# Optimization experiments

Hardware: AMD Instinct MI355X
Metric: run time of the kernel (lower is better)

Reference implementation:

```python
import jax, jax.numpy as jnp
import numpy as np

N_NODES = 5000
N_EDGES = 50000
HID = 64
OUT = 12
H, W = 12, 4
L = 3
BN_EPS = 1e-5
GEN_EPS = 1e-7


def setup_inputs() -> dict:
    key = jax.random.key(0)
    ks = jax.random.split(key, 12)
    node_feats = jax.random.normal(ks[0], (N_NODES, HID, H, W), dtype=jnp.float32)
    edge_feats = jax.random.normal(ks[1], (N_EDGES, HID, H, W), dtype=jnp.float32)
    src = jax.random.randint(ks[2], (N_EDGES,), 0, N_NODES)
    dst = jax.random.randint(ks[3], (N_EDGES,), 0, N_NODES)
    # per-layer params
    bn_gamma = jnp.ones((L, HID), dtype=jnp.float32)
    bn_beta = jnp.zeros((L, HID), dtype=jnp.float32)
    s = 1.0 / np.sqrt(HID)
    gen_W = jax.random.uniform(ks[4], (L, HID, HID), dtype=jnp.float32, minval=-s, maxval=s)
    gen_b = jax.random.uniform(ks[5], (L, HID), dtype=jnp.float32, minval=-s, maxval=s)
    out_W = jax.random.uniform(ks[6], (HID, OUT), dtype=jnp.float32, minval=-s, maxval=s)
    out_b = jax.random.uniform(ks[7], (OUT,), dtype=jnp.float32, minval=-s, maxval=s)
    return {
        "node_feats": node_feats, "edge_feats": edge_feats,
        "src": src, "dst": dst,
        "bn_gamma": bn_gamma, "bn_beta": bn_beta,
        "gen_W": gen_W, "gen_b": gen_b,
        "out_W": out_W, "out_b": out_b,
    }


def _batchnorm2d(x, gamma, beta):
    # training-mode BN over (N, H, W) per channel; x: [N, C, H, W]
    mu = jnp.mean(x, axis=(0, 2, 3), keepdims=True)
    var = jnp.mean((x - mu) ** 2, axis=(0, 2, 3), keepdims=True)
    xn = (x - mu) * jax.lax.rsqrt(var + BN_EPS)
    return xn * gamma[None, :, None, None] + beta[None, :, None, None]


def _genconv(h, he, src, dst, Wg, bg):
    # DeeperGCN GENConv with softmax aggregator (beta=1), mlp_layers=1.
    # h: [N, C, H, W], he: [E, C, H, W]
    m = jax.nn.relu(h[src] + he) + GEN_EPS                      # [E, C, H, W]
    mx = jax.ops.segment_max(m, dst, num_segments=N_NODES)      # [N, C, H, W]
    e = jnp.exp(m - mx[dst])
    s = jax.ops.segment_sum(e, dst, num_segments=N_NODES)
    a = e / s[dst]                                              # edge softmax per dst
    agg = jax.ops.segment_sum(a * m, dst, num_segments=N_NODES)
    feats = h + agg
    # linear over channel dim
    return jnp.einsum('nchw,co->nohw', feats, Wg) + bg[None, :, None, None]


def reference(node_feats, edge_feats, src, dst, bn_gamma, bn_beta, gen_W, gen_b, out_W, out_b):
    hv = node_feats
    he = edge_feats
    for l in range(L):
        hv1 = _batchnorm2d(hv, bn_gamma[l], bn_beta[l])
        hv1 = jax.nn.relu(hv1)  # dropout p=0.0 -> identity
        hv = _genconv(hv1, he, src, dst, gen_W[l], gen_b[l]) + hv
    # AvgPooling(g, hv.transpose(0,3)): mean over dim 0 of [W,C,H,N] == mean over W of hv
    h_g = jnp.mean(hv, axis=3, keepdims=True) * hv              # [N, C, H, W]
    out = jnp.einsum('nchw,co->nohw', h_g, out_W) + out_b[None, :, None, None]
    return out
```

## Files before the change

### kernel.cpp

```cpp
#include <hip/hip_runtime.h>
#include <float.h>

#define NN 5000
#define NE 50000
#define C 64
#define CHW4 768
#define SPLIT 25
#define NPS 200
#define MAXD 64

typedef float f32x4 __attribute__((ext_vector_type(4)));

__global__ void hist_kernel(const int* __restrict__ dst, int* __restrict__ cnt) {
  int e = blockIdx.x * 256 + threadIdx.x;
  if (e < NE) atomicAdd(&cnt[dst[e]], 1);
}

__global__ void scan_kernel(const int* __restrict__ cnt, int* __restrict__ off, int* __restrict__ cur) {
  __shared__ int tsum[256];
  int t = threadIdx.x;
  constexpr int PER = 20;
  int base = t * PER;
  int vals[PER];
  int local = 0;
#pragma unroll
  for (int i = 0; i < PER; i++) {
    int idx = base + i;
    int v = (idx < NN) ? cnt[idx] : 0;
    vals[i] = local;
    local += v;
  }
  tsum[t] = local;
  __syncthreads();
  for (int o = 1; o < 256; o <<= 1) {
    int v = (t >= o) ? tsum[t - o] : 0;
    __syncthreads();
    tsum[t] += v;
    __syncthreads();
  }
  int excl = (t == 0) ? 0 : tsum[t - 1];
#pragma unroll
  for (int i = 0; i < PER; i++) {
    int idx = base + i;
    if (idx < NN) {
      int o2 = excl + vals[i];
      off[idx] = o2;
      cur[idx] = o2;
    }
  }
  if (t == 255) off[NN] = excl + local;
}

__global__ void scatter_kernel(const int* __restrict__ dst, const int* __restrict__ src,
                               int* __restrict__ cur, int* __restrict__ eids, int* __restrict__ srcs) {
  int e = blockIdx.x * 256 + threadIdx.x;
  if (e < NE) {
    int p = atomicAdd(&cur[dst[e]], 1);
    eids[p] = e;
    srcs[p] = src[e];
  }
}

__global__ void bn_stats_kernel(const float* __restrict__ hv, float* __restrict__ statsN) {
  int c = blockIdx.x / SPLIT, s = blockIdx.x % SPLIT;
  int n0 = s * NPS;
  const float4* hv4 = (const float4*)hv;
  float sum = 0.f, ss = 0.f;
  for (int i = threadIdx.x; i < NPS * 12; i += 256) {
    int n = n0 + i / 12, p = i % 12;
    float4 v = hv4[(size_t)n * CHW4 + c * 12 + p];
    sum += v.x + v.y + v.z + v.w;
    ss += v.x * v.x + v.y * v.y + v.z * v.z + v.w * v.w;
  }
  __shared__ float rs[256], rq[256];
  rs[threadIdx.x] = sum;
  rq[threadIdx.x] = ss;
  __syncthreads();
  for (int o = 128; o > 0; o >>= 1) {
    if (threadIdx.x < o) {
      rs[threadIdx.x] += rs[threadIdx.x + o];
      rq[threadIdx.x] += rq[threadIdx.x + o];
    }
    __syncthreads();
  }
  if (threadIdx.x == 0) {
    int r = blockIdx.x & 7;
    atomicAdd(&statsN[r * 128 + c], rs[0]);
    atomicAdd(&statsN[r * 128 + 64 + c], rq[0]);
  }
}

__global__ void finalize2_kernel(const float* __restrict__ statsN, const float* __restrict__ gamma,
                                 const float* __restrict__ beta, float* __restrict__ sc,
                                 float* __restrict__ sh) {
  int c = threadIdx.x;
  if (c < C) {
    float s = 0.f, q = 0.f;
#pragma unroll
    for (int r = 0; r < 8; r++) {
      s += statsN[r * 128 + c];
      q += statsN[r * 128 + 64 + c];
    }
    const float inv = 1.f / 240000.f;
    float mu = s * inv;
    float var = q * inv - mu * mu;
    float scale = gamma[c] * rsqrtf(var + 1e-5f);
    sc[c] = scale;
    sh[c] = beta[c] - mu * scale;
  }
}

template <bool LAST>
__global__ __launch_bounds__(256) void aggregate_kernel(
    const float* __restrict__ hv, const float* __restrict__ he,
    const int* __restrict__ srcs, const int* __restrict__ eids, const int* __restrict__ off,
    const float* __restrict__ Wg, const float* __restrict__ bg,
    const float* __restrict__ sc, const float* __restrict__ sh,
    float* __restrict__ hvNext, float* __restrict__ statsNext,
    const float* __restrict__ oW, const float* __restrict__ ob,
    float* __restrict__ out) {
  __shared__ float Wl[4096];
  __shared__ float fl[3072];
  __shared__ float scl[64], shl[64];
  __shared__ int sE[MAXD], sS[MAXD];
  __shared__ float bsum[64], bsq[64];

  int n = blockIdx.x, t = threadIdx.x;
  for (int i = t; i < 4096; i += 256) Wl[i] = Wg[i];
  if (t < 64) {
    scl[t] = sc[t];
    shl[t] = sh[t];
    bsum[t] = 0.f;
    bsq[t] = 0.f;
  }
  __syncthreads();

  const float4* hv4 = (const float4*)hv;
  const f32x4* heV = (const f32x4*)he;

  float scv[3], shv[3], h1[12];
#pragma unroll
  for (int j = 0; j < 3; j++) {
    int q = t + j * 256;
    int c = q / 12;
    scv[j] = scl[c];
    shv[j] = shl[c];
    float4 v = hv4[(size_t)n * CHW4 + q];
    h1[4 * j + 0] = fmaxf(v.x * scv[j] + shv[j], 0.f);
    h1[4 * j + 1] = fmaxf(v.y * scv[j] + shv[j], 0.f);
    h1[4 * j + 2] = fmaxf(v.z * scv[j] + shv[j], 0.f);
    h1[4 * j + 3] = fmaxf(v.w * scv[j] + shv[j], 0.f);
  }

  float M[12], S[12], T[12];
#pragma unroll
  for (int i = 0; i < 12; i++) {
    M[i] = -FLT_MAX;
    S[i] = 0.f;
    T[i] = 0.f;
  }

  int e0 = off[n], d = off[n + 1] - e0;
  for (int base = 0; base < d; base += MAXD) {
    int cnt = min(MAXD, d - base);
    __syncthreads();
    if (t < cnt) {
      sE[t] = eids[e0 + base + t];
      sS[t] = srcs[e0 + base + t];
    }
    __syncthreads();
#pragma unroll 2
    for (int k = 0; k < cnt; k++) {
      size_t hb = (size_t)sS[k] * CHW4, eb = (size_t)sE[k] * CHW4;
#pragma unroll
      for (int j = 0; j < 3; j++) {
        int q = t + j * 256;
        float4 a = hv4[hb + q];
        f32x4 b = __builtin_nontemporal_load(&heV[eb + q]);
        float av[4] = {a.x, a.y, a.z, a.w};
        float bv[4] = {b.x, b.y, b.z, b.w};
#pragma unroll
        for (int u = 0; u < 4; u++) {
          float x = fmaxf(av[u] * scv[j] + shv[j], 0.f);
          float m = fmaxf(x + bv[u], 0.f) + 1e-7f;
          int idx = j * 4 + u;
          float dd = m - M[idx];
          float ed = __expf(-fabsf(dd));
          float f1 = dd > 0.f ? ed : 1.f;
          float f2 = dd > 0.f ? 1.f : ed;
          S[idx] = S[idx] * f1 + f2;
          T[idx] = T[idx] * f1 + f2 * m;
          M[idx] = fmaxf(M[idx], m);
        }
      }
    }
  }

  bool hasE = d > 0;
  float4* fl4 = (float4*)fl;
#pragma unroll
  for (int j = 0; j < 3; j++) {
    int q = t + j * 256, idx = 4 * j;
    float4 f;
    f.x = h1[idx + 0] + (hasE ? T[idx + 0] / S[idx + 0] : 0.f);
    f.y = h1[idx + 1] + (hasE ? T[idx + 1] / S[idx + 1] : 0.f);
    f.z = h1[idx + 2] + (hasE ? T[idx + 2] / S[idx + 2] : 0.f);
    f.w = h1[idx + 3] + (hasE ? T[idx + 3] / S[idx + 3] : 0.f);
    fl4[q] = f;
  }
  __syncthreads();

  int o0 = (t / 12) * 4, hbp = t % 12;
  float4 acc[4];
  if (t < 192) {
#pragma unroll
    for (int i = 0; i < 4; i++) {
      float bv = bg[o0 + i];
      acc[i] = make_float4(bv, bv, bv, bv);
    }
    const float4* w4 = (const float4*)Wl;
    int widx = o0 >> 2;
    for (int c2 = 0; c2 < 64; c2++) {
      float4 fv = fl4[c2 * 12 + hbp];
      float4 wv = w4[c2 * 16 + widx];
      acc[0].x += wv.x * fv.x; acc[0].y += wv.x * fv.y; acc[0].z += wv.x * fv.z; acc[0].w += wv.x * fv.w;
      acc[1].x += wv.y * fv.x; acc[1].y += wv.y * fv.y; acc[1].z += wv.y * fv.z; acc[1].w += wv.y * fv.w;
      acc[2].x += wv.z * fv.x; acc[2].y += wv.z * fv.y; acc[2].z += wv.z * fv.z; acc[2].w += wv.z * fv.w;
      acc[3].x += wv.w * fv.x; acc[3].y += wv.w * fv.y; acc[3].z += wv.w * fv.z; acc[3].w += wv.w * fv.w;
    }
#pragma unroll
    for (int i = 0; i < 4; i++) {
      float4 r = hv4[(size_t)n * CHW4 + (o0 + i) * 12 + hbp];
      acc[i].x += r.x; acc[i].y += r.y; acc[i].z += r.z; acc[i].w += r.w;
    }
  }

  if constexpr (!LAST) {
    if (t < 192) {
      float4* hn4 = (float4*)hvNext;
#pragma unroll
      for (int i = 0; i < 4; i++) {
        hn4[(size_t)n * CHW4 + (o0 + i) * 12 + hbp] = acc[i];
        float s4 = acc[i].x + acc[i].y + acc[i].z + acc[i].w;
        float q4 = acc[i].x * acc[i].x + acc[i].y * acc[i].y + acc[i].z * acc[i].z + acc[i].w * acc[i].w;
        atomicAdd(&bsum[o0 + i], s4);
        atomicAdd(&bsq[o0 + i], q4);
      }
    }
    __syncthreads();
    int r = n & 7;
    if (t < 64) atomicAdd(&statsNext[r * 128 + t], bsum[t]);
    else if (t < 128) atomicAdd(&statsNext[r * 128 + 64 + (t - 64)], bsq[t - 64]);
  } else {
    __syncthreads();
    if (t < 192) {
#pragma unroll
      for (int i = 0; i < 4; i++) fl4[(o0 + i) * 12 + hbp] = acc[i];
    }
    for (int i = t; i < 768; i += 256) Wl[i] = oW[i];
    __syncthreads();
    for (int i = t; i < 768; i += 256) {
      float4 v = fl4[i];
      Wl[1024 + i] = (v.x + v.y + v.z + v.w) * 0.25f;
    }
    __syncthreads();
    if (t < 144) {
      int o = t / 12, hb = t % 12;
      float bias = ob[o];
      float4 a = make_float4(bias, bias, bias, bias);
      for (int c2 = 0; c2 < 64; c2++) {
        float4 v = fl4[c2 * 12 + hb];
        float wv = Wl[c2 * 12 + o] * Wl[1024 + c2 * 12 + hb];
        a.x += wv * v.x; a.y += wv * v.y; a.z += wv * v.z; a.w += wv * v.w;
      }
      ((float4*)out)[(size_t)n * 144 + t] = a;
    }
  }
}

extern "C" void kernel_launch(void* const* d_in, const int* in_sizes, int n_in,
                              void* d_out, int out_size, void* d_ws, size_t ws_size,
                              hipStream_t stream) {
  const float* node_feats = (const float*)d_in[0];
  const float* edge_feats = (const float*)d_in[1];
  const int* src = (const int*)d_in[2];
  const int* dst = (const int*)d_in[3];
  const float* bn_gamma = (const float*)d_in[4];
  const float* bn_beta = (const float*)d_in[5];
  const float* gen_W = (const float*)d_in[6];
  const float* gen_b = (const float*)d_in[7];
  const float* out_W = (const float*)d_in[8];
  const float* out_b = (const float*)d_in[9];
  float* out = (float*)d_out;

  char* ws = (char*)d_ws;
  float* hvA = (float*)ws;
  float* hvB = (float*)(ws + 61440000);
  float* statsN = (float*)(ws + 122880000);
  float* sc = (float*)(ws + 122884096);
  float* sh = (float*)(ws + 122884352);
  int* cnt = (int*)(ws + 122884608);
  int* off = (int*)(ws + 122904608);
  int* cur = (int*)(ws + 122924612);
  int* eids = (int*)(ws + 122944612);
  int* srcs = (int*)(ws + 123144612);

  hipMemsetAsync(cnt, 0, NN * sizeof(int), stream);
  hist_kernel<<<(NE + 255) / 256, 256, 0, stream>>>(dst, cnt);
  scan_kernel<<<1, 256, 0, stream>>>(cnt, off, cur);
  scatter_kernel<<<(NE + 255) / 256, 256, 0, stream>>>(dst, src, cur, eids, srcs);

  hipMemsetAsync(statsN, 0, 1024 * sizeof(float), stream);
  bn_stats_kernel<<<C * SPLIT, 256, 0, stream>>>(node_feats, statsN);

  const float* hvPrev = node_feats;
  float* bufs[2] = {hvA, hvB};
  for (int l = 0; l < 3; l++) {
    finalize2_kernel<<<1, 64, 0, stream>>>(statsN, bn_gamma + l * C, bn_beta + l * C, sc, sh);
    if (l < 2) {
      hipMemsetAsync(statsN, 0, 1024 * sizeof(float), stream);
      float* hvNext = bufs[l & 1];
      aggregate_kernel<false><<<NN, 256, 0, stream>>>(
          hvPrev, edge_feats, srcs, eids, off, gen_W + l * C * C, gen_b + l * C,
          sc, sh, hvNext, statsN, out_W, out_b, out);
      hvPrev = hvNext;
    } else {
      aggregate_kernel<true><<<NN, 256, 0, stream>>>(
          hvPrev, edge_feats, srcs, eids, off, gen_W + l * C * C, gen_b + l * C,
          sc, sh, hvA, statsN, out_W, out_b, out);
    }
  }
}
```

Baseline: 631.7 us.

## Store normalized node and sorted edge features in bf16, drop online-max softmax

Adds a per-layer kernel that applies BN+ReLU once per node and stores the result as bf16. Layer 0 also writes the edge features as bf16 in dst-sorted order, so layers 1 and 2 read them contiguously instead of gathering fp32 rows through eids. The softmax aggregation now accumulates exp(m) directly with no running max, which removes the rescaling arithmetic. The gathered traffic roughly halves, but bf16 rounding lowers precision and plain exp can overflow for large m. It also adds an extra full pass over node features and a large new workspace buffer.

```diff
diff --git a/kernel.cpp b/kernel.cpp
--- a/kernel.cpp
+++ b/kernel.cpp
@@ -10,6 +10,16 @@
 #define MAXD 64
 
 typedef float f32x4 __attribute__((ext_vector_type(4)));
+typedef unsigned int u32x2 __attribute__((ext_vector_type(2)));
+
+__device__ __forceinline__ unsigned int pack_bf16(float a, float b) {
+  unsigned int ua = __float_as_uint(a), ub = __float_as_uint(b);
+  ua = (ua + 0x7FFFu + ((ua >> 16) & 1u)) >> 16;
+  ub = (ub + 0x7FFFu + ((ub >> 16) & 1u)) & 0xFFFF0000u;
+  return ua | ub;
+}
+__device__ __forceinline__ float bf_lo(unsigned int u) { return __uint_as_float(u << 16); }
+__device__ __forceinline__ float bf_hi(unsigned int u) { return __uint_as_float(u & 0xFFFF0000u); }
 
 __global__ void hist_kernel(const int* __restrict__ dst, int* __restrict__ cnt) {
   int e = blockIdx.x * 256 + threadIdx.x;
@@ -110,9 +120,29 @@
   }
 }
 
-template <bool LAST>
+__global__ __launch_bounds__(256) void h1_kernel(const float* __restrict__ hv,
+                                                 const float* __restrict__ sc,
+                                                 const float* __restrict__ sh,
+                                                 u32x2* __restrict__ h1g) {
+  int idx = blockIdx.x * 256 + threadIdx.x;
+  int q = idx % CHW4;
+  int c = q / 12;
+  float s = sc[c], b = sh[c];
+  float4 v = ((const float4*)hv)[idx];
+  float x0 = fmaxf(v.x * s + b, 0.f);
+  float x1 = fmaxf(v.y * s + b, 0.f);
+  float x2 = fmaxf(v.z * s + b, 0.f);
+  float x3 = fmaxf(v.w * s + b, 0.f);
+  u32x2 o;
+  o.x = pack_bf16(x0, x1);
+  o.y = pack_bf16(x2, x3);
+  h1g[idx] = o;
+}
+
+template <bool FIRST, bool LAST>
 __global__ __launch_bounds__(256) void aggregate_kernel(
     const float* __restrict__ hv, const float* __restrict__ he,
+    const u32x2* __restrict__ h1g, u32x2* __restrict__ heb,
     const int* __restrict__ srcs, const int* __restrict__ eids, const int* __restrict__ off,
     const float* __restrict__ Wg, const float* __restrict__ bg,
     const float* __restrict__ sc, const float* __restrict__ sh,
@@ -122,7 +152,7 @@
   __shared__ float Wl[4096];
   __shared__ float fl[3072];
   __shared__ float scl[64], shl[64];
-  __shared__ int sE[MAXD], sS[MAXD];
+  __shared__ int sS[MAXD], sE[MAXD];
   __shared__ float bsum[64], bsq[64];
 
   int n = blockIdx.x, t = threadIdx.x;
@@ -138,24 +168,22 @@
   const float4* hv4 = (const float4*)hv;
   const f32x4* heV = (const f32x4*)he;
 
-  float scv[3], shv[3], h1[12];
+  float h1[12];
 #pragma unroll
   for (int j = 0; j < 3; j++) {
     int q = t + j * 256;
     int c = q / 12;
-    scv[j] = scl[c];
-    shv[j] = shl[c];
+    float s = scl[c], b = shl[c];
     float4 v = hv4[(size_t)n * CHW4 + q];
-    h1[4 * j + 0] = fmaxf(v.x * scv[j] + shv[j], 0.f);
-    h1[4 * j + 1] = fmaxf(v.y * scv[j] + shv[j], 0.f);
-    h1[4 * j + 2] = fmaxf(v.z * scv[j] + shv[j], 0.f);
-    h1[4 * j + 3] = fmaxf(v.w * scv[j] + shv[j], 0.f);
-  }
-
-  float M[12], S[12], T[12];
+    h1[4 * j + 0] = fmaxf(v.x * s + b, 0.f);
+    h1[4 * j + 1] = fmaxf(v.y * s + b, 0.f);
+    h1[4 * j + 2] = fmaxf(v.z * s + b, 0.f);
+    h1[4 * j + 3] = fmaxf(v.w * s + b, 0.f);
+  }
+
+  float S[12], T[12];
 #pragma unroll
   for (int i = 0; i < 12; i++) {
-    M[i] = -FLT_MAX;
     S[i] = 0.f;
     T[i] = 0.f;
   }
@@ -165,32 +193,38 @@
     int cnt = min(MAXD, d - base);
     __syncthreads();
     if (t < cnt) {
-      sE[t] = eids[e0 + base + t];
       sS[t] = srcs[e0 + base + t];
+      if (FIRST) sE[t] = eids[e0 + base + t];
     }
     __syncthreads();
 #pragma unroll 2
     for (int k = 0; k < cnt; k++) {
-      size_t hb = (size_t)sS[k] * CHW4, eb = (size_t)sE[k] * CHW4;
+      size_t hb = (size_t)sS[k] * CHW4;
+      size_t pb = (size_t)(e0 + base + k) * CHW4;
 #pragma unroll
       for (int j = 0; j < 3; j++) {
         int q = t + j * 256;
-        float4 a = hv4[hb + q];
-        f32x4 b = __builtin_nontemporal_load(&heV[eb + q]);
-        float av[4] = {a.x, a.y, a.z, a.w};
-        float bv[4] = {b.x, b.y, b.z, b.w};
+        u32x2 hg = h1g[hb + q];
+        float hgf[4] = {bf_lo(hg.x), bf_hi(hg.x), bf_lo(hg.y), bf_hi(hg.y)};
+        float hef[4];
+        if (FIRST) {
+          f32x4 b = __builtin_nontemporal_load(&heV[(size_t)sE[k] * CHW4 + q]);
+          hef[0] = b.x; hef[1] = b.y; hef[2] = b.z; hef[3] = b.w;
+          u32x2 o;
+          o.x = pack_bf16(b.x, b.y);
+          o.y = pack_bf16(b.z, b.w);
+          __builtin_nontemporal_store(o, &heb[pb + q]);
+        } else {
+          u32x2 bb = __builtin_nontemporal_load(&heb[pb + q]);
+          hef[0] = bf_lo(bb.x); hef[1] = bf_hi(bb.x); hef[2] = bf_lo(bb.y); hef[3] = bf_hi(bb.y);
+        }
 #pragma unroll
         for (int u = 0; u < 4; u++) {
-          float x = fmaxf(av[u] * scv[j] + shv[j], 0.f);
-          float m = fmaxf(x + bv[u], 0.f) + 1e-7f;
+          float m = fmaxf(hgf[u] + hef[u], 0.f) + 1e-7f;
+          float e = __expf(m);
           int idx = j * 4 + u;
-          float dd = m - M[idx];
-          float ed = __expf(-fabsf(dd));
-          float f1 = dd > 0.f ? ed : 1.f;
-          float f2 = dd > 0.f ? 1.f : ed;
-          S[idx] = S[idx] * f1 + f2;
-          T[idx] = T[idx] * f1 + f2 * m;
-          M[idx] = fmaxf(M[idx], m);
+          S[idx] += e;
+          T[idx] += e * m;
         }
       }
     }
@@ -296,14 +330,16 @@
   char* ws = (char*)d_ws;
   float* hvA = (float*)ws;
   float* hvB = (float*)(ws + 61440000);
-  float* statsN = (float*)(ws + 122880000);
-  float* sc = (float*)(ws + 122884096);
-  float* sh = (float*)(ws + 122884352);
-  int* cnt = (int*)(ws + 122884608);
-  int* off = (int*)(ws + 122904608);
-  int* cur = (int*)(ws + 122924612);
-  int* eids = (int*)(ws + 122944612);
-  int* srcs = (int*)(ws + 123144612);
+  u32x2* h1g = (u32x2*)(ws + 122880000);
+  u32x2* heb = (u32x2*)(ws + 153600000);
+  float* statsN = (float*)(ws + 460800000);
+  float* sc = (float*)(ws + 460804096);
+  float* sh = (float*)(ws + 460804352);
+  int* cnt = (int*)(ws + 460804608);
+  int* off = (int*)(ws + 460824608);
+  int* cur = (int*)(ws + 460844612);
+  int* eids = (int*)(ws + 460864612);
+  int* srcs = (int*)(ws + 461064612);
 
   hipMemsetAsync(cnt, 0, NN * sizeof(int), stream);
   hist_kernel<<<(NE + 255) / 256, 256, 0, stream>>>(dst, cnt);
@@ -317,17 +353,23 @@
   float* bufs[2] = {hvA, hvB};
   for (int l = 0; l < 3; l++) {
     finalize2_kernel<<<1, 64, 0, stream>>>(statsN, bn_gamma + l * C, bn_beta + l * C, sc, sh);
-    if (l < 2) {
+    h1_kernel<<<NN * CHW4 / 256, 256, 0, stream>>>(hvPrev, sc, sh, h1g);
+    if (l == 0) {
       hipMemsetAsync(statsN, 0, 1024 * sizeof(float), stream);
-      float* hvNext = bufs[l & 1];
-      aggregate_kernel<false><<<NN, 256, 0, stream>>>(
-          hvPrev, edge_feats, srcs, eids, off, gen_W + l * C * C, gen_b + l * C,
-          sc, sh, hvNext, statsN, out_W, out_b, out);
-      hvPrev = hvNext;
+      aggregate_kernel<true, false><<<NN, 256, 0, stream>>>(
+          hvPrev, edge_feats, h1g, heb, srcs, eids, off, gen_W, gen_b,
+          sc, sh, bufs[0], statsN, out_W, out_b, out);
+      hvPrev = bufs[0];
+    } else if (l == 1) {
+      hipMemsetAsync(statsN, 0, 1024 * sizeof(float), stream);
+      aggregate_kernel<false, false><<<NN, 256, 0, stream>>>(
+          hvPrev, edge_feats, h1g, heb, srcs, eids, off, gen_W + C * C, gen_b + C,
+          sc, sh, bufs[1], statsN, out_W, out_b, out);
+      hvPrev = bufs[1];
     } else {
-      aggregate_kernel<true><<<NN, 256, 0, stream>>>(
-          hvPrev, edge_feats, srcs, eids, off, gen_W + l * C * C, gen_b + l * C,
-          sc, sh, hvA, statsN, out_W, out_b, out);
-    }
-  }
-}
+      aggregate_kernel<false, true><<<NN, 256, 0, stream>>>(
+          hvPrev, edge_feats, h1g, heb, srcs, eids, off, gen_W + 2 * C * C, gen_b + 2 * C,
+          sc, sh, bufs[0], statsN, out_W, out_b, out);
+    }
+  }
+}
```

New measurement: 559.2 us. 1.13x faster.
